# Performance work log

Measured on AMD Instinct MI355X. Metric: run time of the kernel, lower is better.

The kernel has to match this reference:

```python
import jax, jax.numpy as jnp
import numpy as np

B, T, D = 2, 4096, 512
H = 8  # heads; head_dim = D // H = 64


def setup_inputs() -> dict:
    key = jax.random.key(0)
    ks = jax.random.split(key, 8)
    s = 0.02
    return {
        "queries": jax.random.normal(ks[0], (B, T, D), jnp.float32),
        "keys": jax.random.normal(ks[1], (B, T, D), jnp.float32),
        "values": jax.random.normal(ks[2], (B, T, D), jnp.float32),
        "Wq": jax.random.normal(ks[3], (D, D), jnp.float32) * s,
        "Wk": jax.random.normal(ks[4], (D, D), jnp.float32) * s,
        "Wv": jax.random.normal(ks[5], (D, D), jnp.float32) * s,
        "Wo": jax.random.normal(ks[6], (D, D), jnp.float32) * s,
        "bo": jnp.zeros((D,), jnp.float32),
    }


def reference(queries, keys, values, Wq, Wk, Wv, Wo, bo):
    # pad_dim = 0 for in_dim=512, n_heads=8, so no padding needed.
    Bq, Tq, _ = queries.shape
    Ts = keys.shape[1]
    hd = D // H
    # torch Linear: x @ W.T
    q = (queries @ Wq.T).reshape(Bq, Tq, H, hd).transpose(0, 2, 1, 3)  # [B,H,T,hd]
    k = (keys @ Wk.T).reshape(Bq, Ts, H, hd).transpose(0, 2, 1, 3)
    v = (values @ Wv.T).reshape(Bq, Ts, H, hd).transpose(0, 2, 1, 3)
    attn = jnp.einsum("bhtd,bhsd->bhts", q, k) / np.sqrt(hd).astype(np.float32)
    attn = jax.nn.softmax(attn, axis=-1)  # [B,H,T,Ts]
    z = jnp.einsum("bhts,bhsd->bhtd", attn, v)
    z = z.transpose(0, 2, 1, 3).reshape(Bq, Tq, D)
    out = z @ Wo.T + bo
    return (out, attn)
```

## Files before the change

kernel.cpp:

```cpp
#include <hip/hip_runtime.h>

typedef __attribute__((ext_vector_type(8))) short bf16x8;
typedef __attribute__((ext_vector_type(8))) unsigned short u16x8;
typedef __attribute__((ext_vector_type(4))) float f32x4;

#define DEVINL __device__ __forceinline__

constexpr int TB = 2;
constexpr int TT = 4096;
constexpr int TD = 512;
constexpr int TH = 8;
constexpr int THD = 64;
constexpr int TM = TB * TT;

DEVINL unsigned short f2b(float f) {
  unsigned u = __builtin_bit_cast(unsigned, f);
  u += 0x7FFFu + ((u >> 16) & 1u);
  return (unsigned short)(u >> 16);
}

DEVINL void lgkm_barrier() {
  asm volatile("s_waitcnt lgkmcnt(0)" ::: "memory");
  __builtin_amdgcn_s_barrier();
  __builtin_amdgcn_sched_barrier(0);
}

template<int MODE>
__global__ __launch_bounds__(256, 2)
void gemm_xwt(const float* __restrict__ X, const float* __restrict__ W,
              unsigned short* __restrict__ Yb, float* __restrict__ Yf,
              const float* __restrict__ bias)
{
  constexpr int K = TD, N = TD;
  __shared__ unsigned short As[128][72];
  __shared__ unsigned short Bs[128][72];

  const int t    = threadIdx.x;
  const int lane = t & 63, w = t >> 6;
  const int fr = lane & 15, fq = lane >> 4;
  const int wr = (w >> 1) * 64, wc = (w & 1) * 64;
  const int bm = blockIdx.x * 128, bn = blockIdx.y * 128;
  const int srow = t >> 1;
  const int skh  = (t & 1) * 32;

  f32x4 acc[4][4];
  #pragma unroll
  for (int i = 0; i < 4; ++i)
    #pragma unroll
    for (int j = 0; j < 4; ++j)
      acc[i][j] = f32x4{0.f, 0.f, 0.f, 0.f};

  for (int k0 = 0; k0 < K; k0 += 64) {
    const float* srcA = X + (size_t)(bm + srow) * K + k0 + skh;
    const float* srcB = W + (size_t)(bn + srow) * K + k0 + skh;
    #pragma unroll
    for (int i = 0; i < 4; ++i) {
      float4 a0 = ((const float4*)srcA)[2 * i];
      float4 a1 = ((const float4*)srcA)[2 * i + 1];
      u16x8 oa = {f2b(a0.x), f2b(a0.y), f2b(a0.z), f2b(a0.w),
                  f2b(a1.x), f2b(a1.y), f2b(a1.z), f2b(a1.w)};
      *(u16x8*)&As[srow][skh + i * 8] = oa;
      float4 b0 = ((const float4*)srcB)[2 * i];
      float4 b1 = ((const float4*)srcB)[2 * i + 1];
      u16x8 ob = {f2b(b0.x), f2b(b0.y), f2b(b0.z), f2b(b0.w),
                  f2b(b1.x), f2b(b1.y), f2b(b1.z), f2b(b1.w)};
      *(u16x8*)&Bs[srow][skh + i * 8] = ob;
    }
    __syncthreads();
    #pragma unroll
    for (int kk = 0; kk < 2; ++kk) {
      bf16x8 af[4], bfv[4];
      #pragma unroll
      for (int i = 0; i < 4; ++i)
        af[i] = *(const bf16x8*)&As[wr + i * 16 + fr][kk * 32 + fq * 8];
      #pragma unroll
      for (int j = 0; j < 4; ++j)
        bfv[j] = *(const bf16x8*)&Bs[wc + j * 16 + fr][kk * 32 + fq * 8];
      #pragma unroll
      for (int i = 0; i < 4; ++i)
        #pragma unroll
        for (int j = 0; j < 4; ++j) {
          if (MODE == 2)
            acc[i][j] = __builtin_amdgcn_mfma_f32_16x16x32_bf16(bfv[i], af[j], acc[i][j], 0, 0, 0);
          else
            acc[i][j] = __builtin_amdgcn_mfma_f32_16x16x32_bf16(af[i], bfv[j], acc[i][j], 0, 0, 0);
        }
    }
    __syncthreads();
  }

  #pragma unroll
  for (int i = 0; i < 4; ++i) {
    #pragma unroll
    for (int j = 0; j < 4; ++j) {
      #pragma unroll
      for (int ii = 0; ii < 4; ++ii) {
        float v = acc[i][j][ii];
        if (MODE == 2) {
          const int Nidx = bn + wc + i * 16 + fq * 4 + ii;
          const int Midx = bm + wr + j * 16 + fr;
          const int h = Nidx >> 6, d = Nidx & (THD - 1);
          const int b = Midx >> 12, tt = Midx & (TT - 1);
          Yb[((size_t)(b * TH + h) * THD + d) * TT + tt] = f2b(v);
        } else {
          const int gm = bm + wr + i * 16 + fq * 4 + ii;
          const int gn = bn + wc + j * 16 + fr;
          if (MODE == 1) Yf[(size_t)gm * N + gn] = v + bias[gn];
          else           Yb[(size_t)gm * N + gn] = f2b(v);
        }
      }
    }
  }
}

__global__ __launch_bounds__(256, 2)
void attn_fused(const unsigned short* __restrict__ Qb,
                const unsigned short* __restrict__ Kb,
                const unsigned short* __restrict__ VTg,
                float* __restrict__ attnO, float* __restrict__ Z)
{
  __shared__ unsigned short Qs[64][72];
  __shared__ unsigned short Ks[2][64][72];
  __shared__ unsigned short VTs[2][64][72];
  __shared__ unsigned short Ps[4][16][72];

  const int t    = threadIdx.x;
  const int lane = t & 63, w = t >> 6;
  const int fr = lane & 15, fq = lane >> 4;
  const int bh = blockIdx.y;
  const int b  = bh >> 3, h = bh & 7;
  const int q0 = blockIdx.x * 64;

  const size_t rowQ  = ((size_t)(b * TT + q0)) * TD + h * THD;
  const size_t rowKV = ((size_t)(b * TT)) * TD + h * THD;
  const size_t vtBase = (size_t)bh * THD * TT;

  const int tr = t >> 2;
  const int tc = (t & 3) * 16;

  auto loadK = [&](int kv0, u16x8& r0, u16x8& r1) {
    const unsigned short* src = Kb + rowKV + (size_t)(kv0 + tr) * TD + tc;
    r0 = *(const u16x8*)src;
    r1 = *(const u16x8*)(src + 8);
  };
  auto loadVT = [&](int kv0, u16x8& r0, u16x8& r1) {
    const unsigned short* src = VTg + vtBase + (size_t)tr * TT + kv0 + tc;
    r0 = *(const u16x8*)src;
    r1 = *(const u16x8*)(src + 8);
  };
  auto writeK = [&](int buf, const u16x8& r0, const u16x8& r1) {
    *(u16x8*)&Ks[buf][tr][tc]     = r0;
    *(u16x8*)&Ks[buf][tr][tc + 8] = r1;
  };
  auto writeVT = [&](int buf, const u16x8& r0, const u16x8& r1) {
    *(u16x8*)&VTs[buf][tr][tc]     = r0;
    *(u16x8*)&VTs[buf][tr][tc + 8] = r1;
  };

  {
    const unsigned short* src = Qb + rowQ + (size_t)tr * TD + tc;
    *(u16x8*)&Qs[tr][tc]     = *(const u16x8*)src;
    *(u16x8*)&Qs[tr][tc + 8] = *(const u16x8*)(src + 8);
  }
  u16x8 kr0, kr1, vr0, vr1;
  loadK(0, kr0, kr1);
  writeK(0, kr0, kr1);
  lgkm_barrier();

  bf16x8 aq[2];
  aq[0] = *(const bf16x8*)&Qs[w * 16 + fr][fq * 8];
  aq[1] = *(const bf16x8*)&Qs[w * 16 + fr][32 + fq * 8];

  constexpr int NT = TT / 64;
  constexpr float SC = 0.125f;

  float lsum[4] = {0.f, 0.f, 0.f, 0.f};
  for (int j = 0; j < NT; ++j) {
    const int cur = j & 1;
    if (j + 1 < NT) loadK((j + 1) * 64, kr0, kr1);
    #pragma unroll
    for (int n = 0; n < 4; ++n) {
      f32x4 s = f32x4{0.f, 0.f, 0.f, 0.f};
      #pragma unroll
      for (int kk = 0; kk < 2; ++kk) {
        bf16x8 bk = *(const bf16x8*)&Ks[cur][n * 16 + fr][kk * 32 + fq * 8];
        s = __builtin_amdgcn_mfma_f32_16x16x32_bf16(aq[kk], bk, s, 0, 0, 0);
      }
      #pragma unroll
      for (int i = 0; i < 4; ++i) lsum[i] += __expf(s[i] * SC);
    }
    if (j + 1 < NT) writeK(cur ^ 1, kr0, kr1);
    lgkm_barrier();
  }
  #pragma unroll
  for (int msk = 1; msk <= 8; msk <<= 1)
    #pragma unroll
    for (int i = 0; i < 4; ++i) lsum[i] += __shfl_xor(lsum[i], msk, 64);
  float rinv[4];
  #pragma unroll
  for (int i = 0; i < 4; ++i) rinv[i] = 1.0f / lsum[i];

  loadK(0, kr0, kr1);
  loadVT(0, vr0, vr1);
  writeK(0, kr0, kr1);
  writeVT(0, vr0, vr1);
  lgkm_barrier();

  f32x4 accz[4];
  #pragma unroll
  for (int n = 0; n < 4; ++n) accz[n] = f32x4{0.f, 0.f, 0.f, 0.f};

  const size_t abase = ((size_t)bh * TT + q0 + w * 16 + fq * 4) * TT + fr;

  for (int j = 0; j < NT; ++j) {
    const int cur = j & 1;
    const int kv0 = j * 64;
    if (j + 1 < NT) {
      loadK((j + 1) * 64, kr0, kr1);
      loadVT((j + 1) * 64, vr0, vr1);
    }
    #pragma unroll
    for (int n = 0; n < 4; ++n) {
      f32x4 s = f32x4{0.f, 0.f, 0.f, 0.f};
      #pragma unroll
      for (int kk = 0; kk < 2; ++kk) {
        bf16x8 bk = *(const bf16x8*)&Ks[cur][n * 16 + fr][kk * 32 + fq * 8];
        s = __builtin_amdgcn_mfma_f32_16x16x32_bf16(aq[kk], bk, s, 0, 0, 0);
      }
      #pragma unroll
      for (int i = 0; i < 4; ++i) {
        float p = __expf(s[i] * SC) * rinv[i];
        __builtin_nontemporal_store(p, &attnO[abase + (size_t)i * TT + kv0 + n * 16]);
        Ps[w][fq * 4 + i][n * 16 + fr] = f2b(p);
      }
    }
    asm volatile("s_waitcnt lgkmcnt(0)" ::: "memory");
    __builtin_amdgcn_sched_barrier(0);
    #pragma unroll
    for (int kk = 0; kk < 2; ++kk) {
      bf16x8 ap = *(const bf16x8*)&Ps[w][fr][kk * 32 + fq * 8];
      #pragma unroll
      for (int n = 0; n < 4; ++n) {
        bf16x8 bv = *(const bf16x8*)&VTs[cur][n * 16 + fr][kk * 32 + fq * 8];
        accz[n] = __builtin_amdgcn_mfma_f32_16x16x32_bf16(ap, bv, accz[n], 0, 0, 0);
      }
    }
    if (j + 1 < NT) {
      writeK(cur ^ 1, kr0, kr1);
      writeVT(cur ^ 1, vr0, vr1);
    }
    lgkm_barrier();
  }

  const size_t zbase = ((size_t)(b * TT + q0 + w * 16 + fq * 4)) * TD + h * THD + fr;
  #pragma unroll
  for (int n = 0; n < 4; ++n)
    #pragma unroll
    for (int i = 0; i < 4; ++i)
      Z[zbase + (size_t)i * TD + n * 16] = accz[n][i];
}

extern "C" void kernel_launch(void* const* d_in, const int* in_sizes, int n_in,
                              void* d_out, int out_size, void* d_ws, size_t ws_size,
                              hipStream_t stream) {
  const float* queries = (const float*)d_in[0];
  const float* keys    = (const float*)d_in[1];
  const float* values  = (const float*)d_in[2];
  const float* Wq = (const float*)d_in[3];
  const float* Wk = (const float*)d_in[4];
  const float* Wv = (const float*)d_in[5];
  const float* Wo = (const float*)d_in[6];
  const float* bo = (const float*)d_in[7];

  float* out  = (float*)d_out;
  float* attn = out + (size_t)TM * TD;

  unsigned short* qb = (unsigned short*)d_ws;
  unsigned short* kb = qb + (size_t)TM * TD;
  unsigned short* vt = kb + (size_t)TM * TD;
  float*          zf = (float*)(vt + (size_t)TM * TD);

  dim3 gg(TM / 128, TD / 128), bb(256);
  gemm_xwt<0><<<gg, bb, 0, stream>>>(queries, Wq, qb, nullptr, nullptr);
  gemm_xwt<0><<<gg, bb, 0, stream>>>(keys,    Wk, kb, nullptr, nullptr);
  gemm_xwt<2><<<gg, bb, 0, stream>>>(values,  Wv, vt, nullptr, nullptr);

  attn_fused<<<dim3(TT / 64, TB * TH), bb, 0, stream>>>(qb, kb, vt, attn, zf);

  gemm_xwt<1><<<gg, bb, 0, stream>>>(zf, Wo, nullptr, out, bo);
}
```

Baseline: 545.4 us.

## Widen attention blocks to 128 queries and transpose score MFMA for row-contiguous stores

```diff
diff --git a/kernel.cpp b/kernel.cpp
--- a/kernel.cpp
+++ b/kernel.cpp
@@ -3,6 +3,7 @@
 typedef __attribute__((ext_vector_type(8))) short bf16x8;
 typedef __attribute__((ext_vector_type(8))) unsigned short u16x8;
 typedef __attribute__((ext_vector_type(4))) float f32x4;
+typedef __attribute__((ext_vector_type(2))) unsigned uint2v;
 
 #define DEVINL __device__ __forceinline__
 
@@ -17,6 +18,12 @@
   unsigned u = __builtin_bit_cast(unsigned, f);
   u += 0x7FFFu + ((u >> 16) & 1u);
   return (unsigned short)(u >> 16);
+}
+
+DEVINL unsigned cvtpk(float lo, float hi) {
+  unsigned r;
+  asm("v_cvt_pk_bf16_f32 %0, %1, %2" : "=v"(r) : "v"(lo), "v"(hi));
+  return r;
 }
 
 DEVINL void lgkm_barrier() {
@@ -113,129 +120,127 @@
   }
 }
 
-__global__ __launch_bounds__(256, 2)
+__global__ __launch_bounds__(512, 4)
 void attn_fused(const unsigned short* __restrict__ Qb,
                 const unsigned short* __restrict__ Kb,
                 const unsigned short* __restrict__ VTg,
                 float* __restrict__ attnO, float* __restrict__ Z)
 {
-  __shared__ unsigned short Qs[64][72];
   __shared__ unsigned short Ks[2][64][72];
   __shared__ unsigned short VTs[2][64][72];
-  __shared__ unsigned short Ps[4][16][72];
+  __shared__ unsigned short Ps[8][16][72];
 
   const int t    = threadIdx.x;
   const int lane = t & 63, w = t >> 6;
   const int fr = lane & 15, fq = lane >> 4;
   const int bh = blockIdx.y;
   const int b  = bh >> 3, h = bh & 7;
-  const int q0 = blockIdx.x * 64;
-
-  const size_t rowQ  = ((size_t)(b * TT + q0)) * TD + h * THD;
-  const size_t rowKV = ((size_t)(b * TT)) * TD + h * THD;
+  const int q0 = blockIdx.x * 128;
+
+  const size_t rowKV  = ((size_t)(b * TT)) * TD + h * THD;
   const size_t vtBase = (size_t)bh * THD * TT;
 
-  const int tr = t >> 2;
-  const int tc = (t & 3) * 16;
-
-  auto loadK = [&](int kv0, u16x8& r0, u16x8& r1) {
-    const unsigned short* src = Kb + rowKV + (size_t)(kv0 + tr) * TD + tc;
-    r0 = *(const u16x8*)src;
-    r1 = *(const u16x8*)(src + 8);
+  const int tr = t >> 3;
+  const int tc = (t & 7) * 8;
+
+  auto loadK = [&](int kv0, u16x8& r) {
+    r = *(const u16x8*)(Kb + rowKV + (size_t)(kv0 + tr) * TD + tc);
   };
-  auto loadVT = [&](int kv0, u16x8& r0, u16x8& r1) {
-    const unsigned short* src = VTg + vtBase + (size_t)tr * TT + kv0 + tc;
-    r0 = *(const u16x8*)src;
-    r1 = *(const u16x8*)(src + 8);
+  auto loadVT = [&](int kv0, u16x8& r) {
+    r = *(const u16x8*)(VTg + vtBase + (size_t)tr * TT + kv0 + tc);
   };
-  auto writeK = [&](int buf, const u16x8& r0, const u16x8& r1) {
-    *(u16x8*)&Ks[buf][tr][tc]     = r0;
-    *(u16x8*)&Ks[buf][tr][tc + 8] = r1;
-  };
-  auto writeVT = [&](int buf, const u16x8& r0, const u16x8& r1) {
-    *(u16x8*)&VTs[buf][tr][tc]     = r0;
-    *(u16x8*)&VTs[buf][tr][tc + 8] = r1;
-  };
-
-  {
-    const unsigned short* src = Qb + rowQ + (size_t)tr * TD + tc;
-    *(u16x8*)&Qs[tr][tc]     = *(const u16x8*)src;
-    *(u16x8*)&Qs[tr][tc + 8] = *(const u16x8*)(src + 8);
-  }
-  u16x8 kr0, kr1, vr0, vr1;
-  loadK(0, kr0, kr1);
-  writeK(0, kr0, kr1);
+  auto writeK  = [&](int buf, const u16x8& r) { *(u16x8*)&Ks[buf][tr][tc]  = r; };
+  auto writeVT = [&](int buf, const u16x8& r) { *(u16x8*)&VTs[buf][tr][tc] = r; };
+
+  const unsigned short* qsrc = Qb + ((size_t)(b * TT + q0 + w * 16 + fr)) * TD + h * THD;
+  bf16x8 aq[2];
+  aq[0] = *(const bf16x8*)(qsrc + fq * 8);
+  aq[1] = *(const bf16x8*)(qsrc + 32 + fq * 8);
+
+  constexpr int NT = TT / 64;
+  constexpr float K2 = 0.18033688011112042f;
+
+  u16x8 kr, vr;
+  loadK(0, kr);
+  writeK(0, kr);
   lgkm_barrier();
 
-  bf16x8 aq[2];
-  aq[0] = *(const bf16x8*)&Qs[w * 16 + fr][fq * 8];
-  aq[1] = *(const bf16x8*)&Qs[w * 16 + fr][32 + fq * 8];
-
-  constexpr int NT = TT / 64;
-  constexpr float SC = 0.125f;
-
-  float lsum[4] = {0.f, 0.f, 0.f, 0.f};
+  float lsum = 0.f;
   for (int j = 0; j < NT; ++j) {
     const int cur = j & 1;
-    if (j + 1 < NT) loadK((j + 1) * 64, kr0, kr1);
+    if (j + 1 < NT) loadK((j + 1) * 64, kr);
+    __builtin_amdgcn_s_setprio(1);
     #pragma unroll
     for (int n = 0; n < 4; ++n) {
       f32x4 s = f32x4{0.f, 0.f, 0.f, 0.f};
       #pragma unroll
       for (int kk = 0; kk < 2; ++kk) {
-        bf16x8 bk = *(const bf16x8*)&Ks[cur][n * 16 + fr][kk * 32 + fq * 8];
-        s = __builtin_amdgcn_mfma_f32_16x16x32_bf16(aq[kk], bk, s, 0, 0, 0);
-      }
-      #pragma unroll
-      for (int i = 0; i < 4; ++i) lsum[i] += __expf(s[i] * SC);
-    }
-    if (j + 1 < NT) writeK(cur ^ 1, kr0, kr1);
+        bf16x8 ak = *(const bf16x8*)&Ks[cur][n * 16 + fr][kk * 32 + fq * 8];
+        s = __builtin_amdgcn_mfma_f32_16x16x32_bf16(ak, aq[kk], s, 0, 0, 0);
+      }
+      #pragma unroll
+      for (int i = 0; i < 4; ++i)
+        lsum += __builtin_amdgcn_exp2f(s[i] * K2);
+    }
+    __builtin_amdgcn_s_setprio(0);
+    if (j + 1 < NT) writeK(cur ^ 1, kr);
     lgkm_barrier();
   }
-  #pragma unroll
-  for (int msk = 1; msk <= 8; msk <<= 1)
-    #pragma unroll
-    for (int i = 0; i < 4; ++i) lsum[i] += __shfl_xor(lsum[i], msk, 64);
-  float rinv[4];
-  #pragma unroll
-  for (int i = 0; i < 4; ++i) rinv[i] = 1.0f / lsum[i];
-
-  loadK(0, kr0, kr1);
-  loadVT(0, vr0, vr1);
-  writeK(0, kr0, kr1);
-  writeVT(0, vr0, vr1);
+  lsum += __shfl_xor(lsum, 16, 64);
+  lsum += __shfl_xor(lsum, 32, 64);
+  const float l2i = -__log2f(lsum);
+
+  loadK(0, kr);
+  loadVT(0, vr);
+  writeK(0, kr);
+  writeVT(0, vr);
   lgkm_barrier();
 
   f32x4 accz[4];
   #pragma unroll
   for (int n = 0; n < 4; ++n) accz[n] = f32x4{0.f, 0.f, 0.f, 0.f};
 
-  const size_t abase = ((size_t)bh * TT + q0 + w * 16 + fq * 4) * TT + fr;
+  float* arow = attnO + ((size_t)bh * TT + q0 + w * 16 + fr) * TT + fq * 4;
 
   for (int j = 0; j < NT; ++j) {
     const int cur = j & 1;
     const int kv0 = j * 64;
     if (j + 1 < NT) {
-      loadK((j + 1) * 64, kr0, kr1);
-      loadVT((j + 1) * 64, vr0, vr1);
-    }
+      loadK((j + 1) * 64, kr);
+      loadVT((j + 1) * 64, vr);
+    }
+    f32x4 sv[4];
+    __builtin_amdgcn_s_setprio(1);
     #pragma unroll
     for (int n = 0; n < 4; ++n) {
       f32x4 s = f32x4{0.f, 0.f, 0.f, 0.f};
       #pragma unroll
       for (int kk = 0; kk < 2; ++kk) {
-        bf16x8 bk = *(const bf16x8*)&Ks[cur][n * 16 + fr][kk * 32 + fq * 8];
-        s = __builtin_amdgcn_mfma_f32_16x16x32_bf16(aq[kk], bk, s, 0, 0, 0);
-      }
-      #pragma unroll
-      for (int i = 0; i < 4; ++i) {
-        float p = __expf(s[i] * SC) * rinv[i];
-        __builtin_nontemporal_store(p, &attnO[abase + (size_t)i * TT + kv0 + n * 16]);
-        Ps[w][fq * 4 + i][n * 16 + fr] = f2b(p);
-      }
+        bf16x8 ak = *(const bf16x8*)&Ks[cur][n * 16 + fr][kk * 32 + fq * 8];
+        s = __builtin_amdgcn_mfma_f32_16x16x32_bf16(ak, aq[kk], s, 0, 0, 0);
+      }
+      sv[n] = s;
+    }
+    __builtin_amdgcn_s_setprio(0);
+    float p[4][4];
+    #pragma unroll
+    for (int n = 0; n < 4; ++n)
+      #pragma unroll
+      for (int i = 0; i < 4; ++i)
+        p[n][i] = __builtin_amdgcn_exp2f(fmaf(sv[n][i], K2, l2i));
+    #pragma unroll
+    for (int n = 0; n < 4; ++n) {
+      f32x4 pv4 = {p[n][0], p[n][1], p[n][2], p[n][3]};
+      __builtin_nontemporal_store(pv4, (f32x4*)(arow + kv0 + n * 16));
+    }
+    #pragma unroll
+    for (int n = 0; n < 4; ++n) {
+      uint2v u = {cvtpk(p[n][0], p[n][1]), cvtpk(p[n][2], p[n][3])};
+      *(uint2v*)&Ps[w][fr][n * 16 + fq * 4] = u;
     }
     asm volatile("s_waitcnt lgkmcnt(0)" ::: "memory");
     __builtin_amdgcn_sched_barrier(0);
+    __builtin_amdgcn_s_setprio(1);
     #pragma unroll
     for (int kk = 0; kk < 2; ++kk) {
       bf16x8 ap = *(const bf16x8*)&Ps[w][fr][kk * 32 + fq * 8];
@@ -245,9 +250,10 @@
         accz[n] = __builtin_amdgcn_mfma_f32_16x16x32_bf16(ap, bv, accz[n], 0, 0, 0);
       }
     }
+    __builtin_amdgcn_s_setprio(0);
     if (j + 1 < NT) {
-      writeK(cur ^ 1, kr0, kr1);
-      writeVT(cur ^ 1, vr0, vr1);
+      writeK(cur ^ 1, kr);
+      writeVT(cur ^ 1, vr);
     }
     lgkm_barrier();
   }
@@ -285,7 +291,7 @@
   gemm_xwt<0><<<gg, bb, 0, stream>>>(keys,    Wk, kb, nullptr, nullptr);
   gemm_xwt<2><<<gg, bb, 0, stream>>>(values,  Wv, vt, nullptr, nullptr);
 
-  attn_fused<<<dim3(TT / 64, TB * TH), bb, 0, stream>>>(qb, kb, vt, attn, zf);
+  attn_fused<<<dim3(TT / 128, TB * TH), dim3(512), 0, stream>>>(qb, kb, vt, attn, zf);
 
   gemm_xwt<1><<<gg, bb, 0, stream>>>(zf, Wo, nullptr, out, bo);
 }
```

Measured after the change: 636.4 us. 16.7% more time.
